# Kernel tuning notes

Measured on AMD Instinct MI355X. Metric: run time of the kernel, lower is better.

## Reference

```python
import jax, jax.numpy as jnp
import numpy as np

N, W, D = 2048, 64, 512
TEMP = 16.0
LN_EPS = 1e-5
NORM_EPS = 1e-12


def layernorm(x, w, b):
    mu = jnp.mean(x, axis=-1, keepdims=True)
    var = jnp.mean(jnp.square(x - mu), axis=-1, keepdims=True)
    return (x - mu) * jax.lax.rsqrt(var + LN_EPS) * w + b


def l2norm(x):
    n = jnp.linalg.norm(x, axis=-1, keepdims=True)
    return x / jnp.maximum(n, NORM_EPS)


def setup_inputs() -> dict:
    key = jax.random.key(0)
    ks = jax.random.split(key, 6)
    q = jax.random.normal(ks[0], (N, D), dtype=jnp.float32)
    cm = jax.random.normal(ks[1], (W, D), dtype=jnp.float32)
    s1 = 1.0 / np.sqrt(2 * D)
    s2 = 1.0 / np.sqrt(D)
    return {
        "query_embeddings": q,
        "class_memories": cm,
        "ln1_w": jnp.ones((2 * D,), jnp.float32),
        "ln1_b": jnp.zeros((2 * D,), jnp.float32),
        "w1": jax.random.uniform(ks[2], (2 * D, D), jnp.float32, -s1, s1),
        "b1": jax.random.uniform(ks[3], (D,), jnp.float32, -s1, s1),
        "w2": jax.random.uniform(ks[4], (D, D), jnp.float32, -s2, s2),
        "b2": jax.random.uniform(ks[5], (D,), jnp.float32, -s2, s2),
        "ln2_w": jnp.ones((D,), jnp.float32),
        "ln2_b": jnp.zeros((D,), jnp.float32),
    }


def reference(query_embeddings, class_memories, ln1_w, ln1_b, w1, b1, w2, b2, ln2_w, ln2_b):
    n, w = query_embeddings.shape[0], class_memories.shape[0]
    q_exp = jnp.broadcast_to(query_embeddings[:, None, :], (n, w, D))   # [N,W,D]
    c_exp = jnp.broadcast_to(class_memories[None, :, :], (n, w, D))     # [N,W,D]
    x = jnp.concatenate([q_exp, c_exp], axis=-1)                        # [N,W,2D]
    h = layernorm(x, ln1_w, ln1_b)
    h = h @ w1 + b1                                                     # [N,W,D]
    h = jax.nn.gelu(h, approximate=False)
    h = h @ w2 + b2                                                     # [N,W,D]
    fused = layernorm(h + q_exp, ln2_w, ln2_b)
    sims = jnp.einsum('nwd,wd->nw', l2norm(fused), l2norm(class_memories))
    return TEMP * sims
```

## Files before the change

### kernel.cpp

```cpp
#include <hip/hip_runtime.h>
#include <cstdint>
#include <cstddef>


#define NQ 2048
#define NWC 64
#define DD 512
#define NCHUNK 19

typedef __attribute__((ext_vector_type(8))) short short8;
typedef __attribute__((ext_vector_type(8))) unsigned short ushort8;
typedef __attribute__((ext_vector_type(4))) float f32x4;

__device__ __forceinline__ unsigned short f2bf(float f) {
  unsigned u = __float_as_uint(f);
  u += 0x7fffu + ((u >> 16) & 1u);
  return (unsigned short)(u >> 16);
}

__device__ __forceinline__ unsigned cvtpk2(float lo, float hi) {
  unsigned r;
  asm("v_cvt_pk_bf16_f32 %0, %1, %2" : "=v"(r) : "v"(lo), "v"(hi));
  return r;
}

__device__ __forceinline__ float bf2f(unsigned short u) {
  return __uint_as_float(((unsigned)u) << 16);
}

__device__ __forceinline__ float gelu_f(float h) {
  float h2 = h * h;
  float z2 = h * fmaf(h2, 0.10295890518f, 2.30221607f);
  float e = exp2f(z2);
  return h * (e * __builtin_amdgcn_rcpf(e + 1.0f));
}

__device__ __forceinline__ float wred(float v) {
#pragma unroll
  for (int m = 1; m < 64; m <<= 1) v += __shfl_xor(v, m, 64);
  return v;
}

__device__ __forceinline__ float sel4(f32x4 v, int r) {
  float x = (r & 1) ? v[1] : v[0];
  float y = (r & 1) ? v[3] : v[2];
  return (r & 2) ? y : x;
}

__global__ __launch_bounds__(256) void k_prep(
    const float* __restrict__ q, const float* __restrict__ cm,
    const float* __restrict__ g1, const float* __restrict__ be1,
    const float* __restrict__ w1, const float* __restrict__ w2,
    const float* __restrict__ g2, const float* __restrict__ be2,
    const float* __restrict__ b2,
    float* __restrict__ Sq, float* __restrict__ SSq, float* __restrict__ qst,
    float* __restrict__ Sc, float* __restrict__ SSc, float* __restrict__ cmhg,
    float* __restrict__ c1, float* __restrict__ c2, float* __restrict__ c3,
    float* __restrict__ Gp, float* __restrict__ Cp, float* __restrict__ V,
    float* __restrict__ gg, float* __restrict__ scal) {
  const int b = blockIdx.x, tid = threadIdx.x;
  const int wv = tid >> 6, l = tid & 63;
  __shared__ float shr[3][4];
  __shared__ float s_inv;

  if (b < 256) {
    f32x4 b20 = *(const f32x4*)(b2 + l * 8);
    f32x4 b21 = *(const f32x4*)(b2 + l * 8 + 4);
    f32x4 g20 = *(const f32x4*)(g2 + l * 8);
    f32x4 g21 = *(const f32x4*)(g2 + l * 8 + 4);
    f32x4 e20 = *(const f32x4*)(be2 + l * 8);
    f32x4 e21 = *(const f32x4*)(be2 + l * 8 + 4);
#pragma unroll
    for (int rr = 0; rr < 2; ++rr) {
      int r = b * 8 + wv * 2 + rr;
      const float* row = q + (size_t)r * DD;
      f32x4 q0 = *(const f32x4*)(row + l * 8);
      f32x4 q1 = *(const f32x4*)(row + l * 8 + 4);
      float s0 = 0, s1 = 0, s2 = 0, s3 = 0, s4 = 0;
#pragma unroll
      for (int i = 0; i < 4; ++i) {
        float v = q0[i]; s0 += v; s1 = fmaf(v, v, s1);
        float qb = v + b20[i], g = g20[i];
        s2 += qb; s3 = fmaf(qb, g * g, s3); s4 = fmaf(qb, g * e20[i], s4);
        v = q1[i]; s0 += v; s1 = fmaf(v, v, s1);
        qb = v + b21[i]; g = g21[i];
        s2 += qb; s3 = fmaf(qb, g * g, s3); s4 = fmaf(qb, g * e21[i], s4);
      }
      s0 = wred(s0); s1 = wred(s1); s2 = wred(s2); s3 = wred(s3); s4 = wred(s4);
      if (l == 0) {
        Sq[r] = s0; SSq[r] = s1;
        qst[r * 4 + 0] = s2; qst[r * 4 + 1] = s3; qst[r * 4 + 2] = s4;
      }
    }
  } else if (b < 320) {
    int w = b - 256;
    const float* row = cm + (size_t)w * DD;
    float sm = 0.f, ss = 0.f;
    for (int c = tid; c < DD; c += 256) { float v = row[c]; sm += v; ss = fmaf(v, v, ss); }
    sm = wred(sm); ss = wred(ss);
    if (l == 0) { shr[0][wv] = sm; shr[1][wv] = ss; }
    __syncthreads();
    if (tid == 0) {
      float smt = shr[0][0] + shr[0][1] + shr[0][2] + shr[0][3];
      float sst = shr[1][0] + shr[1][1] + shr[1][2] + shr[1][3];
      Sc[w] = smt; SSc[w] = sst;
      s_inv = 1.0f / fmaxf(sqrtf(sst), 1e-12f);
    }
    __syncthreads();
    float inv = s_inv;
    float a = 0.f, bs = 0.f, d = 0.f;
    for (int c = tid; c < DD; c += 256) {
      float ch = row[c] * inv;
      float gv = g2[c];
      float gch = gv * ch;
      cmhg[(size_t)w * DD + c] = gch;
      a += gch;
      bs = fmaf(be2[c], ch, bs);
      d = fmaf(b2[c], gch, d);
    }
    a = wred(a); bs = wred(bs); d = wred(d);
    __syncthreads();
    if (l == 0) { shr[0][wv] = a; shr[1][wv] = bs; shr[2][wv] = d; }
    __syncthreads();
    if (tid == 0) {
      c1[w] = shr[0][0] + shr[0][1] + shr[0][2] + shr[0][3];
      c2[w] = shr[1][0] + shr[1][1] + shr[1][2] + shr[1][3];
      c3[w] = shr[2][0] + shr[2][1] + shr[2][2] + shr[2][3];
    }
  } else if (b < 336) {
    int bk = b - 320, k0 = bk * 64;
#pragma unroll
    for (int jh = 0; jh < 2; ++jh) {
      int j = tid + jh * 256;
      float g = 0.f, c = 0.f;
#pragma unroll 4
      for (int k = 0; k < 64; ++k) {
        float wv4 = w1[(size_t)(k0 + k) * DD + j];
        g = fmaf(g1[k0 + k], wv4, g);
        c = fmaf(be1[k0 + k], wv4, c);
      }
      Gp[(size_t)bk * DD + j] = g;
      Cp[(size_t)bk * DD + j] = c;
    }
  } else if (b < 400) {
    int bb = b - 336;
    f32x4 g20 = *(const f32x4*)(g2 + l * 8);
    f32x4 g21 = *(const f32x4*)(g2 + l * 8 + 4);
    f32x4 e20 = *(const f32x4*)(be2 + l * 8);
    f32x4 e21 = *(const f32x4*)(be2 + l * 8 + 4);
#pragma unroll
    for (int rr = 0; rr < 2; ++rr) {
      int k = bb * 8 + wv * 2 + rr;
      const float* row = w2 + (size_t)k * DD;
      f32x4 w0 = *(const f32x4*)(row + l * 8);
      f32x4 w1v = *(const f32x4*)(row + l * 8 + 4);
      float s1 = 0, s3 = 0, s4 = 0;
#pragma unroll
      for (int i = 0; i < 4; ++i) {
        float w = w0[i], g = g20[i];
        s1 += w; s3 = fmaf(w, g * g, s3); s4 = fmaf(w, g * e20[i], s4);
        w = w1v[i]; g = g21[i];
        s1 += w; s3 = fmaf(w, g * g, s3); s4 = fmaf(w, g * e21[i], s4);
      }
      s1 = wred(s1); s3 = wred(s3); s4 = wred(s4);
      if (l == 0) {
        V[k * 4 + 0] = s1; V[k * 4 + 1] = s3; V[k * 4 + 2] = s4; V[k * 4 + 3] = 0.f;
      }
    }
  } else {
    float a0 = 0, a1 = 0, a2 = 0;
    for (int c = tid; c < DD; c += 256) {
      float g = g2[c], be = be2[c];
      gg[c] = g * g;
      a0 = fmaf(g, g, a0); a1 = fmaf(g, be, a1); a2 = fmaf(be, be, a2);
    }
    a0 = wred(a0); a1 = wred(a1); a2 = wred(a2);
    if (l == 0) { shr[0][wv] = a0; shr[1][wv] = a1; shr[2][wv] = a2; }
    __syncthreads();
    if (tid == 0) {
      scal[0] = shr[0][0] + shr[0][1] + shr[0][2] + shr[0][3];
      scal[1] = shr[1][0] + shr[1][1] + shr[1][2] + shr[1][3];
      scal[2] = shr[2][0] + shr[2][1] + shr[2][2] + shr[2][3];
    }
  }
}

__global__ __launch_bounds__(512) void k_pack1(
    const float* __restrict__ w1, const float* __restrict__ ln1w,
    const float* __restrict__ cmhg,
    unsigned short* __restrict__ PW1T, unsigned short* __restrict__ PW1B,
    unsigned short* __restrict__ PCT) {
  int b = blockIdx.x;
  if (b < 128) {
    int roff = (b < 64) ? 0 : 512;
    unsigned short* out = (b < 64) ? PW1T : PW1B;
    int tid = (b & 63) * 512 + threadIdx.x;
    int l = tid & 63, t = (tid >> 6) & 15, ct = tid >> 10, g = l >> 4;
    int col = (ct << 4) + (l & 15);
    ushort8 o;
#pragma unroll
    for (int i = 0; i < 8; ++i) {
      int k = t * 32 + g * 8 + i;
      o[i] = f2bf(w1[(size_t)(roff + k) * DD + col] * ln1w[roff + k]);
    }
    *(ushort8*)(out + (size_t)tid * 8) = o;
  } else {
    int tid = (b - 128) * 512 + threadIdx.x;
    int l = tid & 63, t = (tid >> 6) & 15, g = l >> 4;
    int col = ((tid >> 10) << 4) + (l & 15);
    ushort8 o;
#pragma unroll
    for (int i = 0; i < 8; ++i) {
      int k = t * 32 + g * 8 + i;
      o[i] = f2bf(cmhg[(size_t)col * DD + k]);
    }
    *(ushort8*)(PCT + (size_t)tid * 8) = o;
  }
}

__global__ __launch_bounds__(256) void k_gemms(
    const float* __restrict__ q, const float* __restrict__ cm,
    const float* __restrict__ w2,
    const unsigned short* __restrict__ PW1T, const unsigned short* __restrict__ PW1B,
    const unsigned short* __restrict__ PCT,
    float* __restrict__ A, unsigned short* __restrict__ Bwb,
    float* __restrict__ QC, float* __restrict__ M6) {
  int b = blockIdx.x;
  const float* X; const unsigned short* PW; void* Out;
  int bx, by, ostride, obf;
  if (b < 256)      { X = q;  PW = PW1T; Out = A;    bx = b & 7;   by = b >> 3;  ostride = DD;  obf = 0; }
  else if (b < 264) { X = cm; PW = PW1B; Out = Bwb;  bx = b - 256; by = 0;       ostride = DD;  obf = 1; }
  else if (b < 296) { X = q;  PW = PCT;  Out = QC;   bx = 0;       by = b - 264; ostride = NWC; obf = 0; }
  else              { X = w2; PW = PCT;  Out = M6;   bx = 0;       by = b - 296; ostride = NWC; obf = 0; }

  int l = threadIdx.x & 63;
  int wv = threadIdx.x >> 6;
  int lr = l & 15, g = l >> 4;
  int r0 = by * 64 + wv * 16;
  int cb0 = bx * 4;
  f32x4 acc[4] = {{0,0,0,0},{0,0,0,0},{0,0,0,0},{0,0,0,0}};
  const float* xrow = X + (size_t)(r0 + lr) * DD;
#pragma unroll
  for (int t = 0; t < 16; ++t) {
    int kb = t * 32 + g * 8;
    f32x4 x0 = *(const f32x4*)(xrow + kb);
    f32x4 x1 = *(const f32x4*)(xrow + kb + 4);
    union { short8 s; unsigned u[4]; } af;
    af.u[0] = cvtpk2(x0[0], x0[1]);
    af.u[1] = cvtpk2(x0[2], x0[3]);
    af.u[2] = cvtpk2(x1[0], x1[1]);
    af.u[3] = cvtpk2(x1[2], x1[3]);
#pragma unroll
    for (int c = 0; c < 4; ++c) {
      short8 bf = *(const short8*)(PW + (size_t)(((cb0 + c) * 16 + t) * 64 + l) * 8);
      acc[c] = __builtin_amdgcn_mfma_f32_16x16x32_bf16(af.s, bf, acc[c], 0, 0, 0);
    }
  }
#pragma unroll
  for (int c = 0; c < 4; ++c)
#pragma unroll
    for (int r = 0; r < 4; ++r) {
      size_t idx = (size_t)(r0 + g * 4 + r) * ostride + (cb0 + c) * 16 + lr;
      float v = acc[c][r];
      if (obf) ((unsigned short*)Out)[idx] = f2bf(v);
      else     ((float*)Out)[idx] = v;
    }
}

__global__ __launch_bounds__(512) void k_pack2(
    const float* __restrict__ w2, const float* __restrict__ M6,
    const float* __restrict__ V, const unsigned short* __restrict__ Bwb,
    const float* __restrict__ Gp, const float* __restrict__ Cp,
    const float* __restrict__ b1,
    unsigned short* __restrict__ PW2X, unsigned short* __restrict__ PBw,
    float* __restrict__ G, float* __restrict__ C) {
  int b = blockIdx.x;
  if (b < 76) {
    int tid = b * 512 + threadIdx.x;
    int l = tid & 63, t = (tid >> 6) & 15, ct = tid >> 10, g = l >> 4;
    int col = (ct << 4) + (l & 15);
    ushort8 o;
#pragma unroll
    for (int i = 0; i < 8; ++i) {
      int k = t * 32 + g * 8 + i;
      float v;
      if (col < 512)      v = w2[(size_t)k * DD + col];
      else if (col < 576) v = M6[(size_t)k * 64 + (col - 512)];
      else { int cv = col - 576; v = (cv < 3) ? V[k * 4 + cv] : 0.f; }
      o[i] = f2bf(v);
    }
    *(ushort8*)(PW2X + (size_t)tid * 8) = o;
  } else if (b < 84) {
    int tid = (b - 76) * 512 + threadIdx.x;
    int l = tid & 63, t = (tid >> 6) & 15, wt = tid >> 10;
    ushort8 o;
#pragma unroll
    for (int i = 0; i < 8; ++i)
      o[i] = Bwb[(size_t)(wt * 16 + (l & 15)) * DD + t * 32 + (l >> 4) * 8 + i];
    *(ushort8*)(PBw + (size_t)tid * 8) = o;
  } else {
    int c = threadIdx.x;
    float g = 0.f, cc = 0.f;
#pragma unroll
    for (int p = 0; p < 16; ++p) { g += Gp[p * DD + c]; cc += Cp[p * DD + c]; }
    G[c] = g; C[c] = cc + b1[c];
  }
}


__device__ __forceinline__ void async16(const void* g, void* lds) {
  __builtin_amdgcn_global_load_lds(
      (const __attribute__((address_space(1))) void*)(uintptr_t)g,
      (__attribute__((address_space(3))) void*)(unsigned int)(uintptr_t)lds,
      16, 0, 0);
}

__global__ __launch_bounds__(256, 2) void k_main(
    const float* __restrict__ Afull, const unsigned short* __restrict__ PBw,
    const float* __restrict__ G, const float* __restrict__ Cc,
    const float* __restrict__ q, const float* __restrict__ b2,
    const float* __restrict__ gg, const float* __restrict__ qst,
    const float* __restrict__ QC, const float* __restrict__ c1v,
    const float* __restrict__ c2v, const float* __restrict__ c3v,
    const float* __restrict__ Sq, const float* __restrict__ SSq,
    const float* __restrict__ Sc, const float* __restrict__ SSc,
    const float* __restrict__ scal, const unsigned short* __restrict__ PW2X,
    float* __restrict__ out) {

  __shared__ __align__(16) float sG[DD], sC[DD], sGG[DD];
  __shared__ __align__(16) float sA[2][DD], sQB[2][DD];
  __shared__ __align__(16) unsigned short sW[2][16384];

  const int tid = threadIdx.x;
  const int wv = tid >> 6, l = tid & 63;
  const int g = l >> 4, lr = l & 15;
  const int n0 = blockIdx.x * 2;
  const int sub = wv >> 1;
  const int n = n0 + sub;
  const int whalf = wv & 1;
  const int w0 = whalf * 32 + lr;
  const int w1p = w0 + 16;

  sG[tid] = G[tid]; sG[tid + 256] = G[tid + 256];
  sC[tid] = Cc[tid]; sC[tid + 256] = Cc[tid + 256];
  sGG[tid] = gg[tid]; sGG[tid + 256] = gg[tid + 256];
#pragma unroll
  for (int s = 0; s < 2; ++s) {
    sA[s][tid]       = Afull[(size_t)(n0 + s) * DD + tid];
    sA[s][tid + 256] = Afull[(size_t)(n0 + s) * DD + tid + 256];
    sQB[s][tid]       = q[(size_t)(n0 + s) * DD + tid] + b2[tid];
    sQB[s][tid + 256] = q[(size_t)(n0 + s) * DD + tid + 256] + b2[tid + 256];
  }
#pragma unroll
  for (int j = 0; j < 8; ++j)
    async16(PW2X + (size_t)(j * 256 + tid) * 8, &sW[0][(j * 256 + wv * 64) * 8]);

  __syncthreads();

  float sqn = Sq[n], ssqn = SSq[n];
  float mu0 = (sqn + Sc[w0]) * (1.0f / 1024.0f);
  float rs0 = rsqrtf((ssqn + SSc[w0]) * (1.0f / 1024.0f) - mu0 * mu0 + 1e-5f);
  float mu1 = (sqn + Sc[w1p]) * (1.0f / 1024.0f);
  float rs1 = rsqrtf((ssqn + SSc[w1p]) * (1.0f / 1024.0f) - mu1 * mu1 + 1e-5f);
  float al0 = rs0, bl0 = -rs0 * mu0;
  float al1 = rs1, bl1 = -rs1 * mu1;

  short8 af0[16], af1[16];
  const unsigned short* pb0 = PBw + (size_t)(whalf * 2) * 16 * 512;
  const unsigned short* pb1 = PBw + (size_t)(whalf * 2 + 1) * 16 * 512;
#pragma unroll
  for (int t = 0; t < 16; ++t) {
    int kb = t * 32 + g * 8;
    f32x4 a0 = *(const f32x4*)&sA[sub][kb];
    f32x4 a1 = *(const f32x4*)&sA[sub][kb + 4];
    f32x4 g0 = *(const f32x4*)&sG[kb];
    f32x4 g1v = *(const f32x4*)&sG[kb + 4];
    f32x4 c0 = *(const f32x4*)&sC[kb];
    f32x4 c1f = *(const f32x4*)&sC[kb + 4];
    ushort8 ub0 = *(const ushort8*)(pb0 + (size_t)(t * 64 + l) * 8);
    ushort8 ub1 = *(const ushort8*)(pb1 + (size_t)(t * 64 + l) * 8);
    float hA[8], hB[8];
#pragma unroll
    for (int i = 0; i < 4; ++i) {
      float in0 = fmaf(bl0, g0[i], c0[i]);
      float in1 = fmaf(bl1, g0[i], c0[i]);
      hA[i] = gelu_f(fmaf(al0, a0[i] + bf2f(ub0[i]), in0));
      hB[i] = gelu_f(fmaf(al1, a0[i] + bf2f(ub1[i]), in1));
      float jn0 = fmaf(bl0, g1v[i], c1f[i]);
      float jn1 = fmaf(bl1, g1v[i], c1f[i]);
      hA[4 + i] = gelu_f(fmaf(al0, a1[i] + bf2f(ub0[4 + i]), jn0));
      hB[4 + i] = gelu_f(fmaf(al1, a1[i] + bf2f(ub1[4 + i]), jn1));
    }
    union { short8 s; unsigned u[4]; } pa, pb;
    pa.u[0] = cvtpk2(hA[0], hA[1]); pa.u[1] = cvtpk2(hA[2], hA[3]);
    pa.u[2] = cvtpk2(hA[4], hA[5]); pa.u[3] = cvtpk2(hA[6], hA[7]);
    pb.u[0] = cvtpk2(hB[0], hB[1]); pb.u[1] = cvtpk2(hB[2], hB[3]);
    pb.u[2] = cvtpk2(hB[4], hB[5]); pb.u[3] = cvtpk2(hB[6], hB[7]);
    af0[t] = pa.s; af1[t] = pb.s;
  }

  float S20 = 0.f, S50 = 0.f, S21 = 0.f, S51 = 0.f;
  float m6d0 = 0.f, m6d1 = 0.f;
  float v1d0 = 0.f, v3d0 = 0.f, v4d0 = 0.f;
  float v1d1 = 0.f, v3d1 = 0.f, v4d1 = 0.f;

  for (int cc = 0; cc < NCHUNK; ++cc) {
    __syncthreads();
    if (cc < NCHUNK - 1) {
      const unsigned short* src = PW2X + (size_t)(cc + 1) * 16384;
      unsigned short* dst = sW[(cc + 1) & 1];
#pragma unroll
      for (int j = 0; j < 8; ++j)
        async16(src + (size_t)(j * 256 + tid) * 8, &dst[(j * 256 + wv * 64) * 8]);
    }
    const unsigned short* wbuf = sW[cc & 1];

    if (cc < 16) {
      f32x4 acc00 = {0,0,0,0}, acc01 = {0,0,0,0}, acc10 = {0,0,0,0}, acc11 = {0,0,0,0};
#pragma unroll
      for (int t = 0; t < 16; ++t) {
        short8 bf0 = *(const short8*)(wbuf + (size_t)((t * 64 + l) * 8));
        short8 bf1 = *(const short8*)(wbuf + (size_t)(((16 + t) * 64 + l) * 8));
        acc00 = __builtin_amdgcn_mfma_f32_16x16x32_bf16(bf0, af0[t], acc00, 0, 0, 0);
        acc10 = __builtin_amdgcn_mfma_f32_16x16x32_bf16(bf0, af1[t], acc10, 0, 0, 0);
        acc01 = __builtin_amdgcn_mfma_f32_16x16x32_bf16(bf1, af0[t], acc01, 0, 0, 0);
        acc11 = __builtin_amdgcn_mfma_f32_16x16x32_bf16(bf1, af1[t], acc11, 0, 0, 0);
      }
#pragma unroll
      for (int ct = 0; ct < 2; ++ct) {
        int cb = cc * 32 + ct * 16 + g * 4;
        f32x4 qb4 = *(const f32x4*)&sQB[sub][cb];
        f32x4 gg4 = *(const f32x4*)&sGG[cb];
        f32x4 aAv = ct ? acc01 : acc00;
        f32x4 aBv = ct ? acc11 : acc10;
#pragma unroll
        for (int r = 0; r < 4; ++r) {
          float y = aAv[r] + qb4[r];
          float y2 = y * y;
          S20 += y2; S50 = fmaf(y2, gg4[r], S50);
          float z = aBv[r] + qb4[r];
          float z2 = z * z;
          S21 += z2; S51 = fmaf(z2, gg4[r], S51);
        }
      }
    } else if (cc == 16 + whalf) {
      f32x4 acc00 = {0,0,0,0}, acc11 = {0,0,0,0};
#pragma unroll
      for (int t = 0; t < 16; ++t) {
        short8 bf0 = *(const short8*)(wbuf + (size_t)((t * 64 + l) * 8));
        short8 bf1 = *(const short8*)(wbuf + (size_t)(((16 + t) * 64 + l) * 8));
        acc00 = __builtin_amdgcn_mfma_f32_16x16x32_bf16(bf0, af0[t], acc00, 0, 0, 0);
        acc11 = __builtin_amdgcn_mfma_f32_16x16x32_bf16(bf1, af1[t], acc11, 0, 0, 0);
      }
      float d0 = sel4(acc00, lr & 3);
      float d1 = sel4(acc11, lr & 3);
      int src = lr + ((lr >> 2) << 4);
      m6d0 = __shfl(d0, src, 64);
      m6d1 = __shfl(d1, src, 64);
    } else if (cc == 18) {
      f32x4 acc00 = {0,0,0,0}, acc10 = {0,0,0,0};
#pragma unroll
      for (int t = 0; t < 16; ++t) {
        short8 bf0 = *(const short8*)(wbuf + (size_t)((t * 64 + l) * 8));
        acc00 = __builtin_amdgcn_mfma_f32_16x16x32_bf16(bf0, af0[t], acc00, 0, 0, 0);
        acc10 = __builtin_amdgcn_mfma_f32_16x16x32_bf16(bf0, af1[t], acc10, 0, 0, 0);
      }
      v1d0 = __shfl(acc00[0], lr, 64);
      v3d0 = __shfl(acc00[1], lr, 64);
      v4d0 = __shfl(acc00[2], lr, 64);
      v1d1 = __shfl(acc10[0], lr, 64);
      v3d1 = __shfl(acc10[1], lr, 64);
      v4d1 = __shfl(acc10[2], lr, 64);
    }
  }

  S20 += __shfl_xor(S20, 16, 64); S20 += __shfl_xor(S20, 32, 64);
  S50 += __shfl_xor(S50, 16, 64); S50 += __shfl_xor(S50, 32, 64);
  S21 += __shfl_xor(S21, 16, 64); S21 += __shfl_xor(S21, 32, 64);
  S51 += __shfl_xor(S51, 16, 64); S51 += __shfl_xor(S51, 32, 64);

  if (g == 0) {
    float sg2v = scal[0], sgbv = scal[1], sb2v = scal[2];
    float qbs = qst[n * 4 + 0], qggs = qst[n * 4 + 1], qgbs = qst[n * 4 + 2];
#pragma unroll
    for (int p = 0; p < 2; ++p) {
      int w = whalf * 32 + p * 16 + lr;
      float S1 = (p ? v1d1 : v1d0) + qbs;
      float S2 = (p ? S21 : S20);
      float S3 = (p ? v3d1 : v3d0) + qggs;
      float S4 = (p ? v4d1 : v4d0) + qgbs;
      float S5 = (p ? S51 : S50);
      float S6 = (p ? m6d1 : m6d0) + QC[(size_t)n * NWC + w] + c3v[w];
      float mu2 = S1 * (1.0f / 512.0f);
      float var2 = S2 * (1.0f / 512.0f) - mu2 * mu2;
      float rs2 = rsqrtf(var2 + 1e-5f);
      float n2 = rs2 * rs2 * (S5 - 2.f * mu2 * S3 + mu2 * mu2 * sg2v)
               + 2.f * rs2 * (S4 - mu2 * sgbv) + sb2v;
      float num = rs2 * (S6 - mu2 * c1v[w]) + c2v[w];
      out[(size_t)n * NWC + w] = 16.0f * num / fmaxf(sqrtf(fmaxf(n2, 0.f)), 1e-12f);
    }
  }
}


extern "C" void kernel_launch(void* const* d_in, const int* in_sizes, int n_in,
                              void* d_out, int out_size, void* d_ws, size_t ws_size,
                              hipStream_t stream) {
  const float* q    = (const float*)d_in[0];
  const float* cm   = (const float*)d_in[1];
  const float* ln1w = (const float*)d_in[2];
  const float* ln1b = (const float*)d_in[3];
  const float* w1   = (const float*)d_in[4];
  const float* b1   = (const float*)d_in[5];
  const float* w2   = (const float*)d_in[6];
  const float* b2   = (const float*)d_in[7];
  const float* ln2w = (const float*)d_in[8];
  const float* ln2b = (const float*)d_in[9];
  float* out = (float*)d_out;

  char* p = (char*)d_ws;
  auto alloc = [&](size_t bytes) { char* r = p; p += (bytes + 255) & ~(size_t)255; return r; };
  float* A     = (float*)alloc((size_t)NQ * DD * 4);
  unsigned short* Bwb = (unsigned short*)alloc((size_t)NWC * DD * 2);
  float* G     = (float*)alloc(DD * 4);
  float* C     = (float*)alloc(DD * 4);
  float* Gp    = (float*)alloc((size_t)16 * DD * 4);
  float* Cp    = (float*)alloc((size_t)16 * DD * 4);
  float* Sq    = (float*)alloc(NQ * 4);
  float* SSq   = (float*)alloc(NQ * 4);
  float* Sc    = (float*)alloc(NWC * 4);
  float* SSc   = (float*)alloc(NWC * 4);
  float* cmhg  = (float*)alloc((size_t)NWC * DD * 4);
  float* c1    = (float*)alloc(NWC * 4);
  float* c2    = (float*)alloc(NWC * 4);
  float* c3    = (float*)alloc(NWC * 4);
  float* gg    = (float*)alloc(DD * 4);
  float* scal  = (float*)alloc(256);
  float* qst   = (float*)alloc((size_t)NQ * 4 * 4);
  float* QC    = (float*)alloc((size_t)NQ * NWC * 4);
  float* M6buf = (float*)alloc((size_t)DD * NWC * 4);
  float* Vbuf  = (float*)alloc((size_t)DD * 4 * 4);
  unsigned short* PW1T = (unsigned short*)alloc((size_t)DD * DD * 2);
  unsigned short* PW1B = (unsigned short*)alloc((size_t)DD * DD * 2);
  unsigned short* PCT  = (unsigned short*)alloc((size_t)DD * NWC * 2);
  unsigned short* PBw  = (unsigned short*)alloc((size_t)NWC * DD * 2);
  unsigned short* PW2X = (unsigned short*)alloc((size_t)NCHUNK * 16384 * 2);

  k_prep<<<401, 256, 0, stream>>>(q, cm, ln1w, ln1b, w1, w2, ln2w, ln2b, b2,
                                  Sq, SSq, qst, Sc, SSc, cmhg, c1, c2, c3,
                                  Gp, Cp, Vbuf, gg, scal);
  k_pack1<<<136, 512, 0, stream>>>(w1, ln1w, cmhg, PW1T, PW1B, PCT);
  k_gemms<<<304, 256, 0, stream>>>(q, cm, w2, PW1T, PW1B, PCT, A, Bwb, QC, M6buf);
  k_pack2<<<85, 512, 0, stream>>>(w2, M6buf, Vbuf, Bwb, Gp, Cp, b1, PW2X, PBw, G, C);
  k_main<<<1024, 256, 0, stream>>>(A, PBw, G, C, q, b2, gg, qst, QC, c1, c2, c3,
                                   Sq, SSq, Sc, SSc, scal, PW2X, out);
}
```

Baseline: 135.3 us.

## Process four queries per block in k_main to reuse streamed W2 tiles

```diff
diff --git a/kernel.cpp b/kernel.cpp
--- a/kernel.cpp
+++ b/kernel.cpp
@@ -315,7 +315,7 @@
       16, 0, 0);
 }
 
-__global__ __launch_bounds__(256, 2) void k_main(
+__global__ __launch_bounds__(256, 1) void k_main(
     const float* __restrict__ Afull, const unsigned short* __restrict__ PBw,
     const float* __restrict__ G, const float* __restrict__ Cc,
     const float* __restrict__ q, const float* __restrict__ b2,
@@ -328,15 +328,16 @@
     float* __restrict__ out) {
 
   __shared__ __align__(16) float sG[DD], sC[DD], sGG[DD];
-  __shared__ __align__(16) float sA[2][DD], sQB[2][DD];
+  __shared__ __align__(16) float sA[4][DD], sQB[4][DD];
   __shared__ __align__(16) unsigned short sW[2][16384];
 
   const int tid = threadIdx.x;
   const int wv = tid >> 6, l = tid & 63;
   const int g = l >> 4, lr = l & 15;
-  const int n0 = blockIdx.x * 2;
-  const int sub = wv >> 1;
-  const int n = n0 + sub;
+  const int n0 = blockIdx.x * 4;
+  const int na = n0 + (wv >> 1) * 2;
+  const int nb = na + 1;
+  const int sa = na - n0, sb = sa + 1;
   const int whalf = wv & 1;
   const int w0 = whalf * 32 + lr;
   const int w1p = w0 + 16;
@@ -345,7 +346,7 @@
   sC[tid] = Cc[tid]; sC[tid + 256] = Cc[tid + 256];
   sGG[tid] = gg[tid]; sGG[tid + 256] = gg[tid + 256];
 #pragma unroll
-  for (int s = 0; s < 2; ++s) {
+  for (int s = 0; s < 4; ++s) {
     sA[s][tid]       = Afull[(size_t)(n0 + s) * DD + tid];
     sA[s][tid + 256] = Afull[(size_t)(n0 + s) * DD + tid + 256];
     sQB[s][tid]       = q[(size_t)(n0 + s) * DD + tid] + b2[tid];
@@ -357,52 +358,81 @@
 
   __syncthreads();
 
-  float sqn = Sq[n], ssqn = SSq[n];
-  float mu0 = (sqn + Sc[w0]) * (1.0f / 1024.0f);
-  float rs0 = rsqrtf((ssqn + SSc[w0]) * (1.0f / 1024.0f) - mu0 * mu0 + 1e-5f);
-  float mu1 = (sqn + Sc[w1p]) * (1.0f / 1024.0f);
-  float rs1 = rsqrtf((ssqn + SSc[w1p]) * (1.0f / 1024.0f) - mu1 * mu1 + 1e-5f);
-  float al0 = rs0, bl0 = -rs0 * mu0;
-  float al1 = rs1, bl1 = -rs1 * mu1;
-
-  short8 af0[16], af1[16];
+  float sqa = Sq[na], ssqa = SSq[na];
+  float sqb = Sq[nb], ssqb = SSq[nb];
+  float sc0 = Sc[w0], ssc0 = SSc[w0];
+  float sc1 = Sc[w1p], ssc1 = SSc[w1p];
+  float muA0 = (sqa + sc0) * (1.0f / 1024.0f);
+  float rsA0 = rsqrtf((ssqa + ssc0) * (1.0f / 1024.0f) - muA0 * muA0 + 1e-5f);
+  float muA1 = (sqa + sc1) * (1.0f / 1024.0f);
+  float rsA1 = rsqrtf((ssqa + ssc1) * (1.0f / 1024.0f) - muA1 * muA1 + 1e-5f);
+  float muB0 = (sqb + sc0) * (1.0f / 1024.0f);
+  float rsB0 = rsqrtf((ssqb + ssc0) * (1.0f / 1024.0f) - muB0 * muB0 + 1e-5f);
+  float muB1 = (sqb + sc1) * (1.0f / 1024.0f);
+  float rsB1 = rsqrtf((ssqb + ssc1) * (1.0f / 1024.0f) - muB1 * muB1 + 1e-5f);
+  float alA0 = rsA0, blA0 = -rsA0 * muA0;
+  float alA1 = rsA1, blA1 = -rsA1 * muA1;
+  float alB0 = rsB0, blB0 = -rsB0 * muB0;
+  float alB1 = rsB1, blB1 = -rsB1 * muB1;
+
+  short8 afA0[16], afA1[16], afB0[16], afB1[16];
   const unsigned short* pb0 = PBw + (size_t)(whalf * 2) * 16 * 512;
   const unsigned short* pb1 = PBw + (size_t)(whalf * 2 + 1) * 16 * 512;
 #pragma unroll
   for (int t = 0; t < 16; ++t) {
     int kb = t * 32 + g * 8;
-    f32x4 a0 = *(const f32x4*)&sA[sub][kb];
-    f32x4 a1 = *(const f32x4*)&sA[sub][kb + 4];
+    f32x4 aA_0 = *(const f32x4*)&sA[sa][kb];
+    f32x4 aA_1 = *(const f32x4*)&sA[sa][kb + 4];
+    f32x4 aB_0 = *(const f32x4*)&sA[sb][kb];
+    f32x4 aB_1 = *(const f32x4*)&sA[sb][kb + 4];
     f32x4 g0 = *(const f32x4*)&sG[kb];
     f32x4 g1v = *(const f32x4*)&sG[kb + 4];
     f32x4 c0 = *(const f32x4*)&sC[kb];
     f32x4 c1f = *(const f32x4*)&sC[kb + 4];
     ushort8 ub0 = *(const ushort8*)(pb0 + (size_t)(t * 64 + l) * 8);
     ushort8 ub1 = *(const ushort8*)(pb1 + (size_t)(t * 64 + l) * 8);
-    float hA[8], hB[8];
+    float hA0[8], hA1[8], hB0[8], hB1[8];
 #pragma unroll
     for (int i = 0; i < 4; ++i) {
-      float in0 = fmaf(bl0, g0[i], c0[i]);
-      float in1 = fmaf(bl1, g0[i], c0[i]);
-      hA[i] = gelu_f(fmaf(al0, a0[i] + bf2f(ub0[i]), in0));
-      hB[i] = gelu_f(fmaf(al1, a0[i] + bf2f(ub1[i]), in1));
-      float jn0 = fmaf(bl0, g1v[i], c1f[i]);
-      float jn1 = fmaf(bl1, g1v[i], c1f[i]);
-      hA[4 + i] = gelu_f(fmaf(al0, a1[i] + bf2f(ub0[4 + i]), jn0));
-      hB[4 + i] = gelu_f(fmaf(al1, a1[i] + bf2f(ub1[4 + i]), jn1));
-    }
-    union { short8 s; unsigned u[4]; } pa, pb;
-    pa.u[0] = cvtpk2(hA[0], hA[1]); pa.u[1] = cvtpk2(hA[2], hA[3]);
-    pa.u[2] = cvtpk2(hA[4], hA[5]); pa.u[3] = cvtpk2(hA[6], hA[7]);
-    pb.u[0] = cvtpk2(hB[0], hB[1]); pb.u[1] = cvtpk2(hB[2], hB[3]);
-    pb.u[2] = cvtpk2(hB[4], hB[5]); pb.u[3] = cvtpk2(hB[6], hB[7]);
-    af0[t] = pa.s; af1[t] = pb.s;
-  }
-
-  float S20 = 0.f, S50 = 0.f, S21 = 0.f, S51 = 0.f;
-  float m6d0 = 0.f, m6d1 = 0.f;
-  float v1d0 = 0.f, v3d0 = 0.f, v4d0 = 0.f;
-  float v1d1 = 0.f, v3d1 = 0.f, v4d1 = 0.f;
+      float b0lo = bf2f(ub0[i]), b1lo = bf2f(ub1[i]);
+      float b0hi = bf2f(ub0[4 + i]), b1hi = bf2f(ub1[4 + i]);
+      float inA0 = fmaf(blA0, g0[i], c0[i]);
+      float inA1 = fmaf(blA1, g0[i], c0[i]);
+      float inB0 = fmaf(blB0, g0[i], c0[i]);
+      float inB1 = fmaf(blB1, g0[i], c0[i]);
+      hA0[i] = gelu_f(fmaf(alA0, aA_0[i] + b0lo, inA0));
+      hA1[i] = gelu_f(fmaf(alA1, aA_0[i] + b1lo, inA1));
+      hB0[i] = gelu_f(fmaf(alB0, aB_0[i] + b0lo, inB0));
+      hB1[i] = gelu_f(fmaf(alB1, aB_0[i] + b1lo, inB1));
+      float jnA0 = fmaf(blA0, g1v[i], c1f[i]);
+      float jnA1 = fmaf(blA1, g1v[i], c1f[i]);
+      float jnB0 = fmaf(blB0, g1v[i], c1f[i]);
+      float jnB1 = fmaf(blB1, g1v[i], c1f[i]);
+      hA0[4 + i] = gelu_f(fmaf(alA0, aA_1[i] + b0hi, jnA0));
+      hA1[4 + i] = gelu_f(fmaf(alA1, aA_1[i] + b1hi, jnA1));
+      hB0[4 + i] = gelu_f(fmaf(alB0, aB_1[i] + b0hi, jnB0));
+      hB1[4 + i] = gelu_f(fmaf(alB1, aB_1[i] + b1hi, jnB1));
+    }
+    union { short8 s; unsigned u[4]; } pA0, pA1, pB0, pB1;
+    pA0.u[0] = cvtpk2(hA0[0], hA0[1]); pA0.u[1] = cvtpk2(hA0[2], hA0[3]);
+    pA0.u[2] = cvtpk2(hA0[4], hA0[5]); pA0.u[3] = cvtpk2(hA0[6], hA0[7]);
+    pA1.u[0] = cvtpk2(hA1[0], hA1[1]); pA1.u[1] = cvtpk2(hA1[2], hA1[3]);
+    pA1.u[2] = cvtpk2(hA1[4], hA1[5]); pA1.u[3] = cvtpk2(hA1[6], hA1[7]);
+    pB0.u[0] = cvtpk2(hB0[0], hB0[1]); pB0.u[1] = cvtpk2(hB0[2], hB0[3]);
+    pB0.u[2] = cvtpk2(hB0[4], hB0[5]); pB0.u[3] = cvtpk2(hB0[6], hB0[7]);
+    pB1.u[0] = cvtpk2(hB1[0], hB1[1]); pB1.u[1] = cvtpk2(hB1[2], hB1[3]);
+    pB1.u[2] = cvtpk2(hB1[4], hB1[5]); pB1.u[3] = cvtpk2(hB1[6], hB1[7]);
+    afA0[t] = pA0.s; afA1[t] = pA1.s;
+    afB0[t] = pB0.s; afB1[t] = pB1.s;
+  }
+
+  float S2A0 = 0.f, S5A0 = 0.f, S2A1 = 0.f, S5A1 = 0.f;
+  float S2B0 = 0.f, S5B0 = 0.f, S2B1 = 0.f, S5B1 = 0.f;
+  float m6A0 = 0.f, m6A1 = 0.f, m6B0 = 0.f, m6B1 = 0.f;
+  float v1A0 = 0.f, v3A0 = 0.f, v4A0 = 0.f;
+  float v1A1 = 0.f, v3A1 = 0.f, v4A1 = 0.f;
+  float v1B0 = 0.f, v3B0 = 0.f, v4B0 = 0.f;
+  float v1B1 = 0.f, v3B1 = 0.f, v4B1 = 0.f;
 
   for (int cc = 0; cc < NCHUNK; ++cc) {
     __syncthreads();
@@ -416,81 +446,103 @@
     const unsigned short* wbuf = sW[cc & 1];
 
     if (cc < 16) {
-      f32x4 acc00 = {0,0,0,0}, acc01 = {0,0,0,0}, acc10 = {0,0,0,0}, acc11 = {0,0,0,0};
+      f32x4 accA0_0 = {0,0,0,0}, accA0_1 = {0,0,0,0};
+      f32x4 accA1_0 = {0,0,0,0}, accA1_1 = {0,0,0,0};
+      f32x4 accB0_0 = {0,0,0,0}, accB0_1 = {0,0,0,0};
+      f32x4 accB1_0 = {0,0,0,0}, accB1_1 = {0,0,0,0};
 #pragma unroll
       for (int t = 0; t < 16; ++t) {
         short8 bf0 = *(const short8*)(wbuf + (size_t)((t * 64 + l) * 8));
         short8 bf1 = *(const short8*)(wbuf + (size_t)(((16 + t) * 64 + l) * 8));
-        acc00 = __builtin_amdgcn_mfma_f32_16x16x32_bf16(bf0, af0[t], acc00, 0, 0, 0);
-        acc10 = __builtin_amdgcn_mfma_f32_16x16x32_bf16(bf0, af1[t], acc10, 0, 0, 0);
-        acc01 = __builtin_amdgcn_mfma_f32_16x16x32_bf16(bf1, af0[t], acc01, 0, 0, 0);
-        acc11 = __builtin_amdgcn_mfma_f32_16x16x32_bf16(bf1, af1[t], acc11, 0, 0, 0);
+        accA0_0 = __builtin_amdgcn_mfma_f32_16x16x32_bf16(bf0, afA0[t], accA0_0, 0, 0, 0);
+        accA1_0 = __builtin_amdgcn_mfma_f32_16x16x32_bf16(bf0, afA1[t], accA1_0, 0, 0, 0);
+        accB0_0 = __builtin_amdgcn_mfma_f32_16x16x32_bf16(bf0, afB0[t], accB0_0, 0, 0, 0);
+        accB1_0 = __builtin_amdgcn_mfma_f32_16x16x32_bf16(bf0, afB1[t], accB1_0, 0, 0, 0);
+        accA0_1 = __builtin_amdgcn_mfma_f32_16x16x32_bf16(bf1, afA0[t], accA0_1, 0, 0, 0);
+        accA1_1 = __builtin_amdgcn_mfma_f32_16x16x32_bf16(bf1, afA1[t], accA1_1, 0, 0, 0);
+        accB0_1 = __builtin_amdgcn_mfma_f32_16x16x32_bf16(bf1, afB0[t], accB0_1, 0, 0, 0);
+        accB1_1 = __builtin_amdgcn_mfma_f32_16x16x32_bf16(bf1, afB1[t], accB1_1, 0, 0, 0);
       }
 #pragma unroll
       for (int ct = 0; ct < 2; ++ct) {
         int cb = cc * 32 + ct * 16 + g * 4;
-        f32x4 qb4 = *(const f32x4*)&sQB[sub][cb];
+        f32x4 qbA = *(const f32x4*)&sQB[sa][cb];
+        f32x4 qbB = *(const f32x4*)&sQB[sb][cb];
         f32x4 gg4 = *(const f32x4*)&sGG[cb];
-        f32x4 aAv = ct ? acc01 : acc00;
-        f32x4 aBv = ct ? acc11 : acc10;
+        f32x4 aA0 = ct ? accA0_1 : accA0_0;
+        f32x4 aA1 = ct ? accA1_1 : accA1_0;
+        f32x4 aB0 = ct ? accB0_1 : accB0_0;
+        f32x4 aB1 = ct ? accB1_1 : accB1_0;
 #pragma unroll
         for (int r = 0; r < 4; ++r) {
-          float y = aAv[r] + qb4[r];
-          float y2 = y * y;
-          S20 += y2; S50 = fmaf(y2, gg4[r], S50);
-          float z = aBv[r] + qb4[r];
-          float z2 = z * z;
-          S21 += z2; S51 = fmaf(z2, gg4[r], S51);
+          float y, y2;
+          y = aA0[r] + qbA[r]; y2 = y * y; S2A0 += y2; S5A0 = fmaf(y2, gg4[r], S5A0);
+          y = aA1[r] + qbA[r]; y2 = y * y; S2A1 += y2; S5A1 = fmaf(y2, gg4[r], S5A1);
+          y = aB0[r] + qbB[r]; y2 = y * y; S2B0 += y2; S5B0 = fmaf(y2, gg4[r], S5B0);
+          y = aB1[r] + qbB[r]; y2 = y * y; S2B1 += y2; S5B1 = fmaf(y2, gg4[r], S5B1);
         }
       }
     } else if (cc == 16 + whalf) {
-      f32x4 acc00 = {0,0,0,0}, acc11 = {0,0,0,0};
+      f32x4 dA0 = {0,0,0,0}, dA1 = {0,0,0,0}, dB0 = {0,0,0,0}, dB1 = {0,0,0,0};
 #pragma unroll
       for (int t = 0; t < 16; ++t) {
         short8 bf0 = *(const short8*)(wbuf + (size_t)((t * 64 + l) * 8));
         short8 bf1 = *(const short8*)(wbuf + (size_t)(((16 + t) * 64 + l) * 8));
-        acc00 = __builtin_amdgcn_mfma_f32_16x16x32_bf16(bf0, af0[t], acc00, 0, 0, 0);
-        acc11 = __builtin_amdgcn_mfma_f32_16x16x32_bf16(bf1, af1[t], acc11, 0, 0, 0);
-      }
-      float d0 = sel4(acc00, lr & 3);
-      float d1 = sel4(acc11, lr & 3);
+        dA0 = __builtin_amdgcn_mfma_f32_16x16x32_bf16(bf0, afA0[t], dA0, 0, 0, 0);
+        dB0 = __builtin_amdgcn_mfma_f32_16x16x32_bf16(bf0, afB0[t], dB0, 0, 0, 0);
+        dA1 = __builtin_amdgcn_mfma_f32_16x16x32_bf16(bf1, afA1[t], dA1, 0, 0, 0);
+        dB1 = __builtin_amdgcn_mfma_f32_16x16x32_bf16(bf1, afB1[t], dB1, 0, 0, 0);
+      }
       int src = lr + ((lr >> 2) << 4);
-      m6d0 = __shfl(d0, src, 64);
-      m6d1 = __shfl(d1, src, 64);
+      m6A0 = __shfl(sel4(dA0, lr & 3), src, 64);
+      m6A1 = __shfl(sel4(dA1, lr & 3), src, 64);
+      m6B0 = __shfl(sel4(dB0, lr & 3), src, 64);
+      m6B1 = __shfl(sel4(dB1, lr & 3), src, 64);
     } else if (cc == 18) {
-      f32x4 acc00 = {0,0,0,0}, acc10 = {0,0,0,0};
+      f32x4 vA0 = {0,0,0,0}, vA1 = {0,0,0,0}, vB0 = {0,0,0,0}, vB1 = {0,0,0,0};
 #pragma unroll
       for (int t = 0; t < 16; ++t) {
         short8 bf0 = *(const short8*)(wbuf + (size_t)((t * 64 + l) * 8));
-        acc00 = __builtin_amdgcn_mfma_f32_16x16x32_bf16(bf0, af0[t], acc00, 0, 0, 0);
-        acc10 = __builtin_amdgcn_mfma_f32_16x16x32_bf16(bf0, af1[t], acc10, 0, 0, 0);
-      }
-      v1d0 = __shfl(acc00[0], lr, 64);
-      v3d0 = __shfl(acc00[1], lr, 64);
-      v4d0 = __shfl(acc00[2], lr, 64);
-      v1d1 = __shfl(acc10[0], lr, 64);
-      v3d1 = __shfl(acc10[1], lr, 64);
-      v4d1 = __shfl(acc10[2], lr, 64);
-    }
-  }
-
-  S20 += __shfl_xor(S20, 16, 64); S20 += __shfl_xor(S20, 32, 64);
-  S50 += __shfl_xor(S50, 16, 64); S50 += __shfl_xor(S50, 32, 64);
-  S21 += __shfl_xor(S21, 16, 64); S21 += __shfl_xor(S21, 32, 64);
-  S51 += __shfl_xor(S51, 16, 64); S51 += __shfl_xor(S51, 32, 64);
+        vA0 = __builtin_amdgcn_mfma_f32_16x16x32_bf16(bf0, afA0[t], vA0, 0, 0, 0);
+        vA1 = __builtin_amdgcn_mfma_f32_16x16x32_bf16(bf0, afA1[t], vA1, 0, 0, 0);
+        vB0 = __builtin_amdgcn_mfma_f32_16x16x32_bf16(bf0, afB0[t], vB0, 0, 0, 0);
+        vB1 = __builtin_amdgcn_mfma_f32_16x16x32_bf16(bf0, afB1[t], vB1, 0, 0, 0);
+      }
+      v1A0 = __shfl(vA0[0], lr, 64); v3A0 = __shfl(vA0[1], lr, 64); v4A0 = __shfl(vA0[2], lr, 64);
+      v1A1 = __shfl(vA1[0], lr, 64); v3A1 = __shfl(vA1[1], lr, 64); v4A1 = __shfl(vA1[2], lr, 64);
+      v1B0 = __shfl(vB0[0], lr, 64); v3B0 = __shfl(vB0[1], lr, 64); v4B0 = __shfl(vB0[2], lr, 64);
+      v1B1 = __shfl(vB1[0], lr, 64); v3B1 = __shfl(vB1[1], lr, 64); v4B1 = __shfl(vB1[2], lr, 64);
+    }
+  }
+
+  S2A0 += __shfl_xor(S2A0, 16, 64); S2A0 += __shfl_xor(S2A0, 32, 64);
+  S5A0 += __shfl_xor(S5A0, 16, 64); S5A0 += __shfl_xor(S5A0, 32, 64);
+  S2A1 += __shfl_xor(S2A1, 16, 64); S2A1 += __shfl_xor(S2A1, 32, 64);
+  S5A1 += __shfl_xor(S5A1, 16, 64); S5A1 += __shfl_xor(S5A1, 32, 64);
+  S2B0 += __shfl_xor(S2B0, 16, 64); S2B0 += __shfl_xor(S2B0, 32, 64);
+  S5B0 += __shfl_xor(S5B0, 16, 64); S5B0 += __shfl_xor(S5B0, 32, 64);
+  S2B1 += __shfl_xor(S2B1, 16, 64); S2B1 += __shfl_xor(S2B1, 32, 64);
+  S5B1 += __shfl_xor(S5B1, 16, 64); S5B1 += __shfl_xor(S5B1, 32, 64);
 
   if (g == 0) {
     float sg2v = scal[0], sgbv = scal[1], sb2v = scal[2];
-    float qbs = qst[n * 4 + 0], qggs = qst[n * 4 + 1], qgbs = qst[n * 4 + 2];
-#pragma unroll
-    for (int p = 0; p < 2; ++p) {
-      int w = whalf * 32 + p * 16 + lr;
-      float S1 = (p ? v1d1 : v1d0) + qbs;
-      float S2 = (p ? S21 : S20);
-      float S3 = (p ? v3d1 : v3d0) + qggs;
-      float S4 = (p ? v4d1 : v4d0) + qgbs;
-      float S5 = (p ? S51 : S50);
-      float S6 = (p ? m6d1 : m6d0) + QC[(size_t)n * NWC + w] + c3v[w];
+    float qbsA = qst[na * 4 + 0], qggA = qst[na * 4 + 1], qgbA = qst[na * 4 + 2];
+    float qbsB = qst[nb * 4 + 0], qggB = qst[nb * 4 + 1], qgbB = qst[nb * 4 + 2];
+#pragma unroll
+    for (int e = 0; e < 4; ++e) {
+      int n  = (e & 2) ? nb : na;
+      int p  = e & 1;
+      int w  = whalf * 32 + p * 16 + lr;
+      float S1, S2, S3, S4, S5, S6d;
+      if (e == 0)      { S1 = v1A0; S2 = S2A0; S3 = v3A0; S4 = v4A0; S5 = S5A0; S6d = m6A0; }
+      else if (e == 1) { S1 = v1A1; S2 = S2A1; S3 = v3A1; S4 = v4A1; S5 = S5A1; S6d = m6A1; }
+      else if (e == 2) { S1 = v1B0; S2 = S2B0; S3 = v3B0; S4 = v4B0; S5 = S5B0; S6d = m6B0; }
+      else             { S1 = v1B1; S2 = S2B1; S3 = v3B1; S4 = v4B1; S5 = S5B1; S6d = m6B1; }
+      float qbs  = (e & 2) ? qbsB : qbsA;
+      float qggs = (e & 2) ? qggB : qggA;
+      float qgbs = (e & 2) ? qgbB : qgbA;
+      S1 += qbs; S3 += qggs; S4 += qgbs;
+      float S6 = S6d + QC[(size_t)n * NWC + w] + c3v[w];
       float mu2 = S1 * (1.0f / 512.0f);
       float var2 = S2 * (1.0f / 512.0f) - mu2 * mu2;
       float rs2 = rsqrtf(var2 + 1e-5f);
@@ -552,6 +604,6 @@
   k_pack1<<<136, 512, 0, stream>>>(w1, ln1w, cmhg, PW1T, PW1B, PCT);
   k_gemms<<<304, 256, 0, stream>>>(q, cm, w2, PW1T, PW1B, PCT, A, Bwb, QC, M6buf);
   k_pack2<<<85, 512, 0, stream>>>(w2, M6buf, Vbuf, Bwb, Gp, Cp, b1, PW2X, PBw, G, C);
-  k_main<<<1024, 256, 0, stream>>>(A, PBw, G, C, q, b2, gg, qst, QC, c1, c2, c3,
-                                   Sq, SSq, Sc, SSc, scal, PW2X, out);
-}
+  k_main<<<512, 256, 0, stream>>>(A, PBw, G, C, q, b2, gg, qst, QC, c1, c2, c3,
+                                  Sq, SSq, Sc, SSc, scal, PW2X, out);
+}
```

Result: slower. 184.3 us (+36.2%).
